# Kernel tuning notes

Measured on AMD Instinct MI355X. Metric: run time of the kernel, lower is better.

## Reference

```python
import jax, jax.numpy as jnp
import numpy as np

B = 4          # batch
C_FEAT = 32    # shared feature channels
N_PARTS = 24   # body parts
H = 256        # triplane resolution (W = 3*H, three planes concatenated on width)
N_PTS = 8192   # sampled points per batch element
C = C_FEAT + N_PARTS


def setup_inputs() -> dict:
    key = jax.random.key(0)
    k1, k2 = jax.random.split(key)
    triplane = jax.random.normal(k1, (B, C, H, 3 * H), dtype=jnp.float32)
    # canonical coords in [-1, 1], one row per (point, part)
    triplane_coord_3d = jax.random.uniform(
        k2, (B * N_PTS * N_PARTS, 3), dtype=jnp.float32, minval=-1.0, maxval=1.0)
    index = jnp.arange(B * N_PTS, dtype=jnp.int32).reshape(B, N_PTS)
    return {"triplane": triplane, "triplane_coord_3d": triplane_coord_3d, "index": index}


def _bilinear(planes, uv):
    """planes: (B, 3, C, H, H); uv: (B, P, 3, 2) in [-1,1] (x->width, y->height).
    align_corners=False, border-clamped bilinear sample. Returns (B, P, 3, C)."""
    Hs = planes.shape[-1]
    px = (uv[..., 0] + 1.0) * (Hs * 0.5) - 0.5
    py = (uv[..., 1] + 1.0) * (Hs * 0.5) - 0.5
    x0f = jnp.floor(px)
    y0f = jnp.floor(py)
    wx = px - x0f
    wy = py - y0f
    x0 = jnp.clip(x0f.astype(jnp.int32), 0, Hs - 1)
    x1 = jnp.clip(x0f.astype(jnp.int32) + 1, 0, Hs - 1)
    y0 = jnp.clip(y0f.astype(jnp.int32), 0, Hs - 1)
    y1 = jnp.clip(y0f.astype(jnp.int32) + 1, 0, Hs - 1)
    bi = jnp.arange(planes.shape[0])[:, None, None]   # (B,1,1)
    ki = jnp.arange(3)[None, None, :]                 # (1,1,3)

    def g(yi, xi):
        return planes[bi, ki, :, yi, xi]              # (B, P, 3, C)

    return (g(y0, x0) * ((1 - wx) * (1 - wy))[..., None]
            + g(y0, x1) * (wx * (1 - wy))[..., None]
            + g(y1, x0) * ((1 - wx) * wy)[..., None]
            + g(y1, x1) * (wx * wy)[..., None])


def reference(triplane, triplane_coord_3d, index):
    Bq, n = index.shape
    # split width into the 3 concatenated planes -> (B, 3, C, H, H)
    planes = triplane.reshape(Bq, C, H, 3, H).transpose(0, 3, 1, 2, 4)
    # per-(point, part) coordinate rows
    rows = index[..., None] * N_PARTS + jnp.arange(N_PARTS, dtype=index.dtype)  # (B,n,P)
    xyz = triplane_coord_3d[rows]                                 # (B, n, P, 3)
    # plane uv: xy, xz, yz
    uv = jnp.stack([xyz[..., jnp.array([0, 1])],
                    xyz[..., jnp.array([0, 2])],
                    xyz[..., jnp.array([1, 2])]], axis=-2)        # (B, n, P, 3, 2)
    uv = uv.reshape(Bq, n * N_PARTS, 3, 2)
    samp = _bilinear(planes, uv).sum(axis=2)                      # sum over 3 planes -> (B, nP, C)
    samp = samp.reshape(Bq, n, N_PARTS, C)
    part_feature = samp[..., :C_FEAT].mean(axis=-1)               # (B, n, P)
    # part p's probability logit is channel 32+p sampled at part p's coords
    logits = samp[:, :, jnp.arange(N_PARTS), C_FEAT + jnp.arange(N_PARTS)]
    part_prob = jax.nn.softmax(logits, axis=-1)                   # (B, n, P)
    return (part_prob * part_feature).sum(axis=-1)                # (B, n)
```

## Files before the change

### kernel.cpp

```cpp
#include <hip/hip_runtime.h>

#define HS 256
#define W3 768
#define CCH 56
#define CF 32
#define NP 24
#define NPTS 8192
#define NPOINTS (4 * NPTS)
#define PLANE_SZ (HS * W3)

__global__ void tp_mean_kernel(const float* __restrict__ tri,
                               float* __restrict__ M) {
    int i4 = blockIdx.x * blockDim.x + threadIdx.x;
    int b = i4 / (PLANE_SZ / 4);
    int rem = i4 % (PLANE_SZ / 4);
    const float4* in = (const float4*)tri + (size_t)b * CCH * (PLANE_SZ / 4) + rem;
    float4 acc = {0.f, 0.f, 0.f, 0.f};
#pragma unroll
    for (int c = 0; c < CF; ++c) {
        float4 v = in[(size_t)c * (PLANE_SZ / 4)];
        acc.x += v.x; acc.y += v.y; acc.z += v.z; acc.w += v.w;
    }
    const float s = 1.0f / (float)CF;
    acc.x *= s; acc.y *= s; acc.z *= s; acc.w *= s;
    ((float4*)M)[(size_t)b * (PLANE_SZ / 4) + rem] = acc;
}

__global__ void tp_repack_kernel(const float* __restrict__ coords,
                                 const int* __restrict__ index,
                                 float4* __restrict__ Cp) {
    int tid = blockIdx.x * blockDim.x + threadIdx.x;
    int gpoint = tid / NP;
    int part = tid - gpoint * NP;
    int row = index[gpoint] * NP + part;
    float4 v;
    v.x = coords[row * 3 + 0];
    v.y = coords[row * 3 + 1];
    v.z = coords[row * 3 + 2];
    v.w = 0.f;
    Cp[(size_t)part * NPOINTS + gpoint] = v;
}

__device__ __forceinline__ void sample_row(const float* __restrict__ row,
                                           int x0, int x1,
                                           float& c0, float& c1) {
    const int xa = x0 & ~1;
    const float2 v = *reinterpret_cast<const float2*>(row + xa);
    if (x0 & 1) {
        c0 = v.y;
        c1 = (x1 == x0) ? v.y : row[x1];
    } else {
        c0 = v.x;
        c1 = (x1 == x0) ? v.x : v.y;
    }
}

__global__ __launch_bounds__(256) void tp_gather_kernel(
    const float* __restrict__ tri, const float4* __restrict__ Cp,
    const float* __restrict__ M, float* __restrict__ wfeat,
    float* __restrict__ wlog) {
    const int w = (blockIdx.x & 7) * 384 + (blockIdx.x >> 3);
    const int group = w >> 5;
    const int chunk = w & 31;
    const int b = group / NP;
    const int part = group - b * NP;

    const int gpoint = b * NPTS + chunk * 256 + threadIdx.x;

    const float4 c4 = Cp[(size_t)part * NPOINTS + gpoint];
    const float x = c4.x, y = c4.y, z = c4.z;

    const float us[3] = {x, x, y};
    const float vs[3] = {y, z, z};

    const float* __restrict__ Mb = M + (size_t)b * PLANE_SZ;
    const float* __restrict__ Tb = tri + (size_t)(b * CCH + CF + part) * PLANE_SZ;

    float feat = 0.f, lg = 0.f;
#pragma unroll
    for (int k = 0; k < 3; ++k) {
        const float px = (us[k] + 1.0f) * (HS * 0.5f) - 0.5f;
        const float py = (vs[k] + 1.0f) * (HS * 0.5f) - 0.5f;
        const float x0f = floorf(px);
        const float y0f = floorf(py);
        const float wx = px - x0f;
        const float wy = py - y0f;
        const int x0i = (int)x0f;
        const int y0i = (int)y0f;
        const int x0 = min(max(x0i, 0), HS - 1);
        const int x1 = min(max(x0i + 1, 0), HS - 1);
        const int y0 = min(max(y0i, 0), HS - 1);
        const int y1 = min(max(y0i + 1, 0), HS - 1);
        const float w00 = (1.f - wx) * (1.f - wy);
        const float w01 = wx * (1.f - wy);
        const float w10 = (1.f - wx) * wy;
        const float w11 = wx * wy;

        const int r0 = y0 * W3 + k * HS;
        const int r1 = y1 * W3 + k * HS;

        float m00, m01, m10, m11, t00, t01, t10, t11;
        sample_row(Mb + r0, x0, x1, m00, m01);
        sample_row(Mb + r1, x0, x1, m10, m11);
        sample_row(Tb + r0, x0, x1, t00, t01);
        sample_row(Tb + r1, x0, x1, t10, t11);

        feat += m00 * w00 + m01 * w01 + m10 * w10 + m11 * w11;
        lg   += t00 * w00 + t01 * w01 + t10 * w10 + t11 * w11;
    }

    wfeat[(size_t)part * NPOINTS + gpoint] = feat;
    wlog[(size_t)part * NPOINTS + gpoint] = lg;
}

__global__ __launch_bounds__(256) void tp_softmax_kernel(
    const float* __restrict__ wfeat, const float* __restrict__ wlog,
    float* __restrict__ out) {
    const int gpoint = blockIdx.x * 256 + threadIdx.x;
    float f[NP], l[NP];
#pragma unroll
    for (int p = 0; p < NP; ++p) {
        f[p] = wfeat[(size_t)p * NPOINTS + gpoint];
        l[p] = wlog[(size_t)p * NPOINTS + gpoint];
    }
    float mx = -1e30f;
#pragma unroll
    for (int p = 0; p < NP; ++p) mx = fmaxf(mx, l[p]);
    float se = 0.f, acc = 0.f;
#pragma unroll
    for (int p = 0; p < NP; ++p) {
        const float e = __expf(l[p] - mx);
        se += e;
        acc += e * f[p];
    }
    out[gpoint] = acc / se;
}

extern "C" void kernel_launch(void* const* d_in, const int* in_sizes, int n_in,
                              void* d_out, int out_size, void* d_ws, size_t ws_size,
                              hipStream_t stream) {
    const float* tri = (const float*)d_in[0];
    const float* coords = (const float*)d_in[1];
    const int* index = (const int*)d_in[2];
    float* out = (float*)d_out;

    float* M = (float*)d_ws;
    float4* Cp = (float4*)(M + 4 * PLANE_SZ);
    float* wfeat = (float*)(Cp + NP * NPOINTS);
    float* wlog = wfeat + NP * NPOINTS;

    tp_mean_kernel<<<(4 * PLANE_SZ / 4) / 256, 256, 0, stream>>>(tri, M);
    tp_repack_kernel<<<(NPOINTS * NP) / 256, 256, 0, stream>>>(coords, index, Cp);
    tp_gather_kernel<<<3072, 256, 0, stream>>>(tri, Cp, M, wfeat, wlog);
    tp_softmax_kernel<<<NPOINTS / 256, 256, 0, stream>>>(wfeat, wlog, out);
}
```

Before: 326.5 us.

## Interleave mean and logit planes per part to pair gathers, remap gather grid

The mean kernel now also writes, for every (batch, part), an interleaved plane holding the channel mean and that part's logit channel side by side. The gather kernel can then fetch both bilinear corners of both quantities with one float4 load. The gather grid shrinks, with each block looping over three parts, and batches are assigned to XCD pairs for cache locality. In exchange the workspace grows to about 150 MB of interleaved data that must be written each call, which adds a lot of write traffic.

Result: slower. 350.4 us (+7.3%).

```diff
diff --git a/kernel.cpp b/kernel.cpp
--- a/kernel.cpp
+++ b/kernel.cpp
@@ -8,22 +8,33 @@
 #define NPTS 8192
 #define NPOINTS (4 * NPTS)
 #define PLANE_SZ (HS * W3)
+#define PQ (PLANE_SZ / 4)
 
-__global__ void tp_mean_kernel(const float* __restrict__ tri,
-                               float* __restrict__ M) {
-    int i4 = blockIdx.x * blockDim.x + threadIdx.x;
-    int b = i4 / (PLANE_SZ / 4);
-    int rem = i4 % (PLANE_SZ / 4);
-    const float4* in = (const float4*)tri + (size_t)b * CCH * (PLANE_SZ / 4) + rem;
+__global__ __launch_bounds__(256) void tp_fuse_kernel(
+    const float* __restrict__ tri, float* __restrict__ F) {
+    const int t = blockIdx.x * 256 + threadIdx.x;
+    const int b = t / PQ;
+    const int rem = t - b * PQ;
+    const float4* __restrict__ base = (const float4*)tri + (size_t)b * CCH * PQ;
+
     float4 acc = {0.f, 0.f, 0.f, 0.f};
 #pragma unroll
     for (int c = 0; c < CF; ++c) {
-        float4 v = in[(size_t)c * (PLANE_SZ / 4)];
+        float4 v = base[(size_t)c * PQ + rem];
         acc.x += v.x; acc.y += v.y; acc.z += v.z; acc.w += v.w;
     }
     const float s = 1.0f / (float)CF;
     acc.x *= s; acc.y *= s; acc.z *= s; acc.w *= s;
-    ((float4*)M)[(size_t)b * (PLANE_SZ / 4) + rem] = acc;
+
+#pragma unroll
+    for (int p = 0; p < NP; ++p) {
+        const float4 tl = base[(size_t)(CF + p) * PQ + rem];
+        float4* dst = (float4*)(F + ((size_t)(b * NP + p) * PLANE_SZ + 4 * rem) * 2);
+        float4 o0 = {acc.x, tl.x, acc.y, tl.y};
+        float4 o1 = {acc.z, tl.z, acc.w, tl.w};
+        dst[0] = o0;
+        dst[1] = o1;
+    }
 }
 
 __global__ void tp_repack_kernel(const float* __restrict__ coords,
@@ -41,76 +52,78 @@
     Cp[(size_t)part * NPOINTS + gpoint] = v;
 }
 
-__device__ __forceinline__ void sample_row(const float* __restrict__ row,
-                                           int x0, int x1,
-                                           float& c0, float& c1) {
+__device__ __forceinline__ void sample_fused(const float* __restrict__ P,
+                                             int r, int x0, int x1,
+                                             float& m0, float& t0,
+                                             float& m1, float& t1) {
     const int xa = x0 & ~1;
-    const float2 v = *reinterpret_cast<const float2*>(row + xa);
+    const float4 v = *reinterpret_cast<const float4*>(P + 2 * (r + xa));
     if (x0 & 1) {
-        c0 = v.y;
-        c1 = (x1 == x0) ? v.y : row[x1];
+        m0 = v.z; t0 = v.w;
+        if (x1 == x0) { m1 = m0; t1 = t0; }
+        else {
+            const float2 w = *reinterpret_cast<const float2*>(P + 2 * (r + x1));
+            m1 = w.x; t1 = w.y;
+        }
     } else {
-        c0 = v.x;
-        c1 = (x1 == x0) ? v.x : v.y;
+        m0 = v.x; t0 = v.y;
+        if (x1 == x0) { m1 = m0; t1 = t0; }
+        else { m1 = v.z; t1 = v.w; }
     }
 }
 
 __global__ __launch_bounds__(256) void tp_gather_kernel(
-    const float* __restrict__ tri, const float4* __restrict__ Cp,
-    const float* __restrict__ M, float* __restrict__ wfeat,
-    float* __restrict__ wlog) {
-    const int w = (blockIdx.x & 7) * 384 + (blockIdx.x >> 3);
-    const int group = w >> 5;
-    const int chunk = w & 31;
-    const int b = group / NP;
-    const int part = group - b * NP;
-
+    const float* __restrict__ F, const float4* __restrict__ Cp,
+    float* __restrict__ wfeat, float* __restrict__ wlog) {
+    const int xcd = blockIdx.x & 7;
+    const int idx = blockIdx.x >> 3;
+    const int b = xcd >> 1;
+    const int pslot = idx & 3;
+    const int chunk = idx >> 2;
     const int gpoint = b * NPTS + chunk * 256 + threadIdx.x;
 
-    const float4 c4 = Cp[(size_t)part * NPOINTS + gpoint];
-    const float x = c4.x, y = c4.y, z = c4.z;
+    for (int gg = 0; gg < 3; ++gg) {
+        const int part = (xcd & 1) * 12 + gg * 4 + pslot;
+        const float4 c4 = Cp[(size_t)part * NPOINTS + gpoint];
+        const float x = c4.x, y = c4.y, z = c4.z;
+        const float us[3] = {x, x, y};
+        const float vs[3] = {y, z, z};
+        const float* __restrict__ Fp = F + (size_t)(b * NP + part) * PLANE_SZ * 2;
 
-    const float us[3] = {x, x, y};
-    const float vs[3] = {y, z, z};
+        float feat = 0.f, lg = 0.f;
+#pragma unroll
+        for (int k = 0; k < 3; ++k) {
+            const float px = (us[k] + 1.0f) * (HS * 0.5f) - 0.5f;
+            const float py = (vs[k] + 1.0f) * (HS * 0.5f) - 0.5f;
+            const float x0f = floorf(px);
+            const float y0f = floorf(py);
+            const float wx = px - x0f;
+            const float wy = py - y0f;
+            const int x0i = (int)x0f;
+            const int y0i = (int)y0f;
+            const int x0 = min(max(x0i, 0), HS - 1);
+            const int x1 = min(max(x0i + 1, 0), HS - 1);
+            const int y0 = min(max(y0i, 0), HS - 1);
+            const int y1 = min(max(y0i + 1, 0), HS - 1);
+            const float w00 = (1.f - wx) * (1.f - wy);
+            const float w01 = wx * (1.f - wy);
+            const float w10 = (1.f - wx) * wy;
+            const float w11 = wx * wy;
 
-    const float* __restrict__ Mb = M + (size_t)b * PLANE_SZ;
-    const float* __restrict__ Tb = tri + (size_t)(b * CCH + CF + part) * PLANE_SZ;
+            const int r0 = y0 * W3 + k * HS;
+            const int r1 = y1 * W3 + k * HS;
 
-    float feat = 0.f, lg = 0.f;
-#pragma unroll
-    for (int k = 0; k < 3; ++k) {
-        const float px = (us[k] + 1.0f) * (HS * 0.5f) - 0.5f;
-        const float py = (vs[k] + 1.0f) * (HS * 0.5f) - 0.5f;
-        const float x0f = floorf(px);
-        const float y0f = floorf(py);
-        const float wx = px - x0f;
-        const float wy = py - y0f;
-        const int x0i = (int)x0f;
-        const int y0i = (int)y0f;
-        const int x0 = min(max(x0i, 0), HS - 1);
-        const int x1 = min(max(x0i + 1, 0), HS - 1);
-        const int y0 = min(max(y0i, 0), HS - 1);
-        const int y1 = min(max(y0i + 1, 0), HS - 1);
-        const float w00 = (1.f - wx) * (1.f - wy);
-        const float w01 = wx * (1.f - wy);
-        const float w10 = (1.f - wx) * wy;
-        const float w11 = wx * wy;
+            float m00, t00, m01, t01, m10, t10, m11, t11;
+            sample_fused(Fp, r0, x0, x1, m00, t00, m01, t01);
+            sample_fused(Fp, r1, x0, x1, m10, t10, m11, t11);
 
-        const int r0 = y0 * W3 + k * HS;
-        const int r1 = y1 * W3 + k * HS;
+            feat += m00 * w00 + m01 * w01 + m10 * w10 + m11 * w11;
+            lg   += t00 * w00 + t01 * w01 + t10 * w10 + t11 * w11;
+        }
 
-        float m00, m01, m10, m11, t00, t01, t10, t11;
-        sample_row(Mb + r0, x0, x1, m00, m01);
-        sample_row(Mb + r1, x0, x1, m10, m11);
-        sample_row(Tb + r0, x0, x1, t00, t01);
-        sample_row(Tb + r1, x0, x1, t10, t11);
-
-        feat += m00 * w00 + m01 * w01 + m10 * w10 + m11 * w11;
-        lg   += t00 * w00 + t01 * w01 + t10 * w10 + t11 * w11;
+        wfeat[(size_t)part * NPOINTS + gpoint] = feat;
+        wlog[(size_t)part * NPOINTS + gpoint] = lg;
     }
-
-    wfeat[(size_t)part * NPOINTS + gpoint] = feat;
-    wlog[(size_t)part * NPOINTS + gpoint] = lg;
 }
 
 __global__ __launch_bounds__(256) void tp_softmax_kernel(
@@ -144,13 +157,13 @@
     const int* index = (const int*)d_in[2];
     float* out = (float*)d_out;
 
-    float* M = (float*)d_ws;
-    float4* Cp = (float4*)(M + 4 * PLANE_SZ);
+    float* F = (float*)d_ws;
+    float4* Cp = (float4*)(F + (size_t)4 * NP * PLANE_SZ * 2);
     float* wfeat = (float*)(Cp + NP * NPOINTS);
     float* wlog = wfeat + NP * NPOINTS;
 
-    tp_mean_kernel<<<(4 * PLANE_SZ / 4) / 256, 256, 0, stream>>>(tri, M);
+    tp_fuse_kernel<<<(4 * PQ) / 256, 256, 0, stream>>>(tri, F);
     tp_repack_kernel<<<(NPOINTS * NP) / 256, 256, 0, stream>>>(coords, index, Cp);
-    tp_gather_kernel<<<3072, 256, 0, stream>>>(tri, Cp, M, wfeat, wlog);
+    tp_gather_kernel<<<1024, 256, 0, stream>>>(F, Cp, wfeat, wlog);
     tp_softmax_kernel<<<NPOINTS / 256, 256, 0, stream>>>(wfeat, wlog, out);
 }
```
